# Performance work log

Hardware: AMD Instinct MI355X
Metric: run time of the kernel (lower is better)

The kernel has to match this reference:

```python
import jax, jax.numpy as jnp
import numpy as np

N_QUBITS = 10
CNOT_CHAIN = [(i, i + 1) for i in range(N_QUBITS - 1)] + [(N_QUBITS - 1, 0)]


def setup_inputs() -> dict:
    key = jax.random.key(0)
    k1, k2, k3, k4 = jax.random.split(key, 4)
    B, S, E, F = 32, 512, 1024, 4096
    return {
        "x": jax.random.normal(k1, (B, S, N_QUBITS), dtype=jnp.float32),
        "q_params": jax.random.normal(k2, (N_QUBITS,), dtype=jnp.float32),
        "W1": jax.random.normal(k3, (F, N_QUBITS), dtype=jnp.float32) / np.sqrt(N_QUBITS),
        "W2": jax.random.normal(k4, (E, F), dtype=jnp.float32) / np.sqrt(F),
    }


def _simulate(angles):
    """Batched state-vector sim: RX(angle_i) on wire i from |0..0>, CNOT ring,
    then Pauli-Z expectation on every wire. angles: [N, n] -> [N, n]."""
    N, n = angles.shape
    half = 0.5 * angles
    c, s = jnp.cos(half), jnp.sin(half)
    # RX(theta)|0> = [cos(theta/2), -i sin(theta/2)]; per-qubit states [N, n, 2]
    qs = jnp.stack([c.astype(jnp.complex64), (-1j) * s.astype(jnp.complex64)], axis=-1)
    # product state via iterated Kronecker product -> [N, 2^n]
    state = qs[:, 0]
    for i in range(1, n):
        state = (state[:, :, None] * qs[:, i][:, None, :]).reshape(N, -1)
    state = state.reshape((N,) + (2,) * n)  # axis i+1 <-> wire i
    # CNOT(src, tgt): flip target amplitudes on the control=1 half (permutation)
    for src, tgt in CNOT_CHAIN:
        s0, s1 = jnp.split(state, 2, axis=src + 1)
        state = jnp.concatenate([s0, jnp.flip(s1, axis=tgt + 1)], axis=src + 1)
    probs = (state.real ** 2 + state.imag ** 2).reshape(N, -1)  # [N, 2^n]
    # <Z_i> = sum_k p_k * (1 - 2*bit_i(k)); wire 0 is the most-significant bit
    bits = (jnp.arange(2 ** n)[:, None] >> (n - 1 - jnp.arange(n))) & 1
    signs = (1 - 2 * bits).astype(probs.dtype)  # [2^n, n]
    return probs @ signs


def reference(x, q_params, W1, W2):
    B, S, n = x.shape
    # back-to-back RX on the same wire commute: angles add
    angles = (x + q_params).reshape(B * S, n)
    q_out = _simulate(angles).reshape(B, S, n)
    # dropout is identity at inference; it sits before ReLU and is a no-op here
    h = jax.nn.relu(q_out @ W1.T)  # [B, S, ffn_dim]
    return h @ W2.T  # [B, S, embed_dim]
```

## Files before the change

### kernel.cpp

```cpp
#include <hip/hip_runtime.h>
#include <hip/hip_bf16.h>

typedef __bf16 bf16x8 __attribute__((ext_vector_type(8)));
typedef float f32x16 __attribute__((ext_vector_type(16)));

#define NQ     10
#define M_ROWS 16384
#define N_COLS 1024
#define K_DIM  4096

__device__ __forceinline__ void gload_lds16(const __hip_bfloat16* g, __hip_bfloat16* l) {
  __builtin_amdgcn_global_load_lds(
      (const __attribute__((address_space(1))) void*)g,
      (__attribute__((address_space(3))) void*)l,
      16, 0, 0);
}

__global__ void __launch_bounds__(256) prep(const float* __restrict__ W1,
                                            float* __restrict__ W1T,
                                            const float* __restrict__ W2,
                                            __hip_bfloat16* __restrict__ W2b) {
  const int b = blockIdx.x;
  if (b < 4096) {
    int i = (b * 256 + threadIdx.x) * 4;
    float4 v = *(const float4*)(W2 + i);
    union { __hip_bfloat16 h[4]; uint2 u; } p;
    p.h[0] = __float2bfloat16(v.x);
    p.h[1] = __float2bfloat16(v.y);
    p.h[2] = __float2bfloat16(v.z);
    p.h[3] = __float2bfloat16(v.w);
    *(uint2*)(W2b + i) = p.u;
  } else {
    int f = (b - 4096) * 256 + threadIdx.x;
#pragma unroll
    for (int j = 0; j < NQ; j++)
      W1T[j * K_DIM + f] = W1[f * NQ + j];
  }
}

__global__ void __launch_bounds__(256) compute_h(const float* __restrict__ x,
                                                 const float* __restrict__ qp,
                                                 const float* __restrict__ W1T,
                                                 __hip_bfloat16* __restrict__ h) {
  __shared__ float qs[8][NQ];
  const int tid = threadIdx.x;
  const int r0 = blockIdx.x * 8;

  if (tid < 8 * NQ) {
    int r = tid / NQ, j = tid % NQ;
    qs[r][j] = cosf(x[(r0 + r) * NQ + j] + qp[j]);
  }
  __syncthreads();
  if (tid < 8) {
    float c[NQ];
#pragma unroll
    for (int j = 0; j < NQ; j++) c[j] = qs[tid][j];
    float pref = c[0];
    float prod19 = 1.f;
#pragma unroll
    for (int j = 1; j < NQ; j++) prod19 *= c[j];
    qs[tid][0] = prod19;
#pragma unroll
    for (int k = 1; k < NQ; k++) { pref *= c[k]; qs[tid][k] = pref; }
  }
  __syncthreads();

#pragma unroll 1
  for (int k = 0; k < 2; k++) {
    const int col0 = k * 2048 + tid * 8;
    float w[8][NQ];
#pragma unroll
    for (int j = 0; j < NQ; j++) {
      float4 a = *(const float4*)(W1T + j * K_DIM + col0);
      float4 b = *(const float4*)(W1T + j * K_DIM + col0 + 4);
      w[0][j] = a.x; w[1][j] = a.y; w[2][j] = a.z; w[3][j] = a.w;
      w[4][j] = b.x; w[5][j] = b.y; w[6][j] = b.z; w[7][j] = b.w;
    }
#pragma unroll
    for (int r = 0; r < 8; r++) {
      float q[NQ];
#pragma unroll
      for (int j = 0; j < NQ; j++) q[j] = qs[r][j];
      union { __hip_bfloat16 hh[8]; uint4 u; } pk;
#pragma unroll
      for (int c = 0; c < 8; c++) {
        float acc = 0.f;
#pragma unroll
        for (int j = 0; j < NQ; j++) acc = fmaf(q[j], w[c][j], acc);
        pk.hh[c] = __float2bfloat16(fmaxf(acc, 0.f));
      }
      *(uint4*)(h + (r0 + r) * K_DIM + col0) = pk.u;
    }
  }
}

__global__ void __launch_bounds__(256, 2) gemm_bt(const __hip_bfloat16* __restrict__ A,
                                                  const __hip_bfloat16* __restrict__ B,
                                                  float* __restrict__ C) {
  __shared__ __align__(16) __hip_bfloat16 As[256 * 64];
  __shared__ __align__(16) __hip_bfloat16 Bs[128 * 64];

  const int tid  = threadIdx.x;
  const int wave = tid >> 6;
  const int lane = tid & 63;
  const int l31  = lane & 31;
  const int l5   = lane >> 5;
  const int l7   = l31 & 7;
  const int wm   = (wave & 1) * 128;
  const int wn   = (wave >> 1) * 64;

  const int L    = blockIdx.x;
  const int xcd  = L & 7;
  const int idx  = L >> 3;
  const int col0 = (idx >> 3) * 128;
  const int row0 = ((xcd << 3) | (idx & 7)) * 256;

  const int ldrow = lane >> 3;
  const int ldc   = (((lane & 7) ^ ldrow) << 3);

  f32x16 acc[4][2];
#pragma unroll
  for (int i = 0; i < 4; i++)
#pragma unroll
    for (int j = 0; j < 2; j++)
#pragma unroll
      for (int r = 0; r < 16; r++) acc[i][j][r] = 0.f;

  for (int k0 = 0; k0 < K_DIM; k0 += 64) {
#pragma unroll
    for (int i = 0; i < 8; i++)
      gload_lds16(A + (row0 + wave * 64 + i * 8 + ldrow) * K_DIM + k0 + ldc,
                  As + (wave * 8 + i) * 512);
#pragma unroll
    for (int i = 0; i < 4; i++)
      gload_lds16(B + (col0 + wave * 32 + i * 8 + ldrow) * K_DIM + k0 + ldc,
                  Bs + (wave * 4 + i) * 512);
    __syncthreads();

#pragma unroll
    for (int kki = 0; kki < 4; kki++) {
      const int ch = (((2 * kki + l5) ^ l7) << 3);
      bf16x8 af[4], bb[2];
#pragma unroll
      for (int f = 0; f < 4; f++)
        af[f] = *(const bf16x8*)(As + (wm + f * 32 + l31) * 64 + ch);
#pragma unroll
      for (int f = 0; f < 2; f++)
        bb[f] = *(const bf16x8*)(Bs + (wn + f * 32 + l31) * 64 + ch);
#pragma unroll
      for (int fm = 0; fm < 4; fm++)
#pragma unroll
        for (int fn = 0; fn < 2; fn++)
          acc[fm][fn] = __builtin_amdgcn_mfma_f32_32x32x16_bf16(af[fm], bb[fn], acc[fm][fn], 0, 0, 0);
    }
    __syncthreads();
  }

#pragma unroll
  for (int fm = 0; fm < 4; fm++) {
#pragma unroll
    for (int fn = 0; fn < 2; fn++) {
      const int colb = col0 + wn + fn * 32 + l31;
      const int rowb = row0 + wm + fm * 32 + 4 * l5;
#pragma unroll
      for (int reg = 0; reg < 16; reg++) {
        int row = rowb + (reg & 3) + 8 * (reg >> 2);
        C[row * N_COLS + colb] = acc[fm][fn][reg];
      }
    }
  }
}

extern "C" void kernel_launch(void* const* d_in, const int* in_sizes, int n_in,
                              void* d_out, int out_size, void* d_ws, size_t ws_size,
                              hipStream_t stream) {
  const float* x  = (const float*)d_in[0];
  const float* qp = (const float*)d_in[1];
  const float* W1 = (const float*)d_in[2];
  const float* W2 = (const float*)d_in[3];
  float* out = (float*)d_out;

  char* ws = (char*)d_ws;
  float*          W1T = (float*)ws;
  __hip_bfloat16* W2b = (__hip_bfloat16*)(ws + 163840);
  __hip_bfloat16* hbf = (__hip_bfloat16*)(ws + 163840 + 8388608);

  prep<<<4112, 256, 0, stream>>>(W1, W1T, W2, W2b);
  compute_h<<<M_ROWS / 8, 256, 0, stream>>>(x, qp, W1T, hbf);
  gemm_bt<<<(M_ROWS / 256) * (N_COLS / 128), 256, 0, stream>>>(hbf, W2b, out);
}
```

Before: 248.7 us.

## Fuse first-layer projection into GEMM via MFMA, dropping h materialization

Removes the separate compute_h kernel and the 128MB bf16 h buffer. Inside the GEMM, each k-tile of h is recomputed on the fly with an MFMA (W1 padded to K=16 times the quantum features), passed through ReLU, and written swizzled into LDS. The quantum feature computation moves into the prep kernel, which emits padded bf16 Q and W1 arrays. This trades the global write and read of h for redundant recomputation of h across the 8 column blocks and extra MFMA and LDS-write work per k-step.

```diff
diff --git a/kernel.cpp b/kernel.cpp
--- a/kernel.cpp
+++ b/kernel.cpp
@@ -17,12 +17,16 @@
 }
 
 __global__ void __launch_bounds__(256) prep(const float* __restrict__ W1,
-                                            float* __restrict__ W1T,
                                             const float* __restrict__ W2,
-                                            __hip_bfloat16* __restrict__ W2b) {
+                                            const float* __restrict__ x,
+                                            const float* __restrict__ qp,
+                                            __hip_bfloat16* __restrict__ W2b,
+                                            __hip_bfloat16* __restrict__ Wq,
+                                            __hip_bfloat16* __restrict__ Qb) {
   const int b = blockIdx.x;
+  const int tid = threadIdx.x;
   if (b < 4096) {
-    int i = (b * 256 + threadIdx.x) * 4;
+    int i = (b * 256 + tid) * 4;
     float4 v = *(const float4*)(W2 + i);
     union { __hip_bfloat16 h[4]; uint2 u; } p;
     p.h[0] = __float2bfloat16(v.x);
@@ -30,73 +34,42 @@
     p.h[2] = __float2bfloat16(v.z);
     p.h[3] = __float2bfloat16(v.w);
     *(uint2*)(W2b + i) = p.u;
+  } else if (b < 4112) {
+    int kcol = (b - 4096) * 256 + tid;
+    union { __hip_bfloat16 h[16]; uint4 u[2]; } p;
+#pragma unroll
+    for (int j = 0; j < NQ; j++) p.h[j] = __float2bfloat16(W1[kcol * NQ + j]);
+#pragma unroll
+    for (int j = NQ; j < 16; j++) p.h[j] = __float2bfloat16(0.f);
+    *(uint4*)(Wq + kcol * 16) = p.u[0];
+    *(uint4*)(Wq + kcol * 16 + 8) = p.u[1];
   } else {
-    int f = (b - 4096) * 256 + threadIdx.x;
+    int row = (b - 4112) * 256 + tid;
+    float c[NQ];
 #pragma unroll
-    for (int j = 0; j < NQ; j++)
-      W1T[j * K_DIM + f] = W1[f * NQ + j];
+    for (int j = 0; j < NQ; j++) c[j] = cosf(x[row * NQ + j] + qp[j]);
+    float q[NQ];
+    float prod19 = 1.f;
+#pragma unroll
+    for (int j = 1; j < NQ; j++) prod19 *= c[j];
+    q[0] = prod19;
+    float pref = c[0];
+#pragma unroll
+    for (int k = 1; k < NQ; k++) { pref *= c[k]; q[k] = pref; }
+    union { __hip_bfloat16 h[16]; uint4 u[2]; } p;
+#pragma unroll
+    for (int j = 0; j < NQ; j++) p.h[j] = __float2bfloat16(q[j]);
+#pragma unroll
+    for (int j = NQ; j < 16; j++) p.h[j] = __float2bfloat16(0.f);
+    *(uint4*)(Qb + row * 16) = p.u[0];
+    *(uint4*)(Qb + row * 16 + 8) = p.u[1];
   }
 }
 
-__global__ void __launch_bounds__(256) compute_h(const float* __restrict__ x,
-                                                 const float* __restrict__ qp,
-                                                 const float* __restrict__ W1T,
-                                                 __hip_bfloat16* __restrict__ h) {
-  __shared__ float qs[8][NQ];
-  const int tid = threadIdx.x;
-  const int r0 = blockIdx.x * 8;
-
-  if (tid < 8 * NQ) {
-    int r = tid / NQ, j = tid % NQ;
-    qs[r][j] = cosf(x[(r0 + r) * NQ + j] + qp[j]);
-  }
-  __syncthreads();
-  if (tid < 8) {
-    float c[NQ];
-#pragma unroll
-    for (int j = 0; j < NQ; j++) c[j] = qs[tid][j];
-    float pref = c[0];
-    float prod19 = 1.f;
-#pragma unroll
-    for (int j = 1; j < NQ; j++) prod19 *= c[j];
-    qs[tid][0] = prod19;
-#pragma unroll
-    for (int k = 1; k < NQ; k++) { pref *= c[k]; qs[tid][k] = pref; }
-  }
-  __syncthreads();
-
-#pragma unroll 1
-  for (int k = 0; k < 2; k++) {
-    const int col0 = k * 2048 + tid * 8;
-    float w[8][NQ];
-#pragma unroll
-    for (int j = 0; j < NQ; j++) {
-      float4 a = *(const float4*)(W1T + j * K_DIM + col0);
-      float4 b = *(const float4*)(W1T + j * K_DIM + col0 + 4);
-      w[0][j] = a.x; w[1][j] = a.y; w[2][j] = a.z; w[3][j] = a.w;
-      w[4][j] = b.x; w[5][j] = b.y; w[6][j] = b.z; w[7][j] = b.w;
-    }
-#pragma unroll
-    for (int r = 0; r < 8; r++) {
-      float q[NQ];
-#pragma unroll
-      for (int j = 0; j < NQ; j++) q[j] = qs[r][j];
-      union { __hip_bfloat16 hh[8]; uint4 u; } pk;
-#pragma unroll
-      for (int c = 0; c < 8; c++) {
-        float acc = 0.f;
-#pragma unroll
-        for (int j = 0; j < NQ; j++) acc = fmaf(q[j], w[c][j], acc);
-        pk.hh[c] = __float2bfloat16(fmaxf(acc, 0.f));
-      }
-      *(uint4*)(h + (r0 + r) * K_DIM + col0) = pk.u;
-    }
-  }
-}
-
-__global__ void __launch_bounds__(256, 2) gemm_bt(const __hip_bfloat16* __restrict__ A,
-                                                  const __hip_bfloat16* __restrict__ B,
-                                                  float* __restrict__ C) {
+__global__ void __launch_bounds__(256, 2) gemm_fused(const __hip_bfloat16* __restrict__ Qb,
+                                                     const __hip_bfloat16* __restrict__ Wq,
+                                                     const __hip_bfloat16* __restrict__ B,
+                                                     float* __restrict__ C) {
   __shared__ __align__(16) __hip_bfloat16 As[256 * 64];
   __shared__ __align__(16) __hip_bfloat16 Bs[128 * 64];
 
@@ -118,6 +91,11 @@
   const int ldrow = lane >> 3;
   const int ldc   = (((lane & 7) ^ ldrow) << 3);
 
+  bf16x8 qb[2];
+#pragma unroll
+  for (int i = 0; i < 2; i++)
+    qb[i] = *(const bf16x8*)(Qb + (row0 + (2 * wave + i) * 32 + l31) * 16 + l5 * 8);
+
   f32x16 acc[4][2];
 #pragma unroll
   for (int i = 0; i < 4; i++)
@@ -128,13 +106,35 @@
 
   for (int k0 = 0; k0 < K_DIM; k0 += 64) {
 #pragma unroll
-    for (int i = 0; i < 8; i++)
-      gload_lds16(A + (row0 + wave * 64 + i * 8 + ldrow) * K_DIM + k0 + ldc,
-                  As + (wave * 8 + i) * 512);
-#pragma unroll
     for (int i = 0; i < 4; i++)
       gload_lds16(B + (col0 + wave * 32 + i * 8 + ldrow) * K_DIM + k0 + ldc,
                   Bs + (wave * 4 + i) * 512);
+
+    bf16x8 wq[2];
+#pragma unroll
+    for (int kt = 0; kt < 2; kt++)
+      wq[kt] = *(const bf16x8*)(Wq + (k0 + kt * 32 + l31) * 16 + l5 * 8);
+
+#pragma unroll
+    for (int kt = 0; kt < 2; kt++) {
+#pragma unroll
+      for (int i = 0; i < 2; i++) {
+        f32x16 d;
+#pragma unroll
+        for (int r = 0; r < 16; r++) d[r] = 0.f;
+        d = __builtin_amdgcn_mfma_f32_32x32x16_bf16(wq[kt], qb[i], d, 0, 0, 0);
+        const int hrow = (2 * wave + i) * 32 + l31;
+#pragma unroll
+        for (int q = 0; q < 4; q++) {
+          union { __hip_bfloat16 h[4]; ushort4 u; } p;
+#pragma unroll
+          for (int r = 0; r < 4; r++)
+            p.h[r] = __float2bfloat16(fmaxf(d[4 * q + r], 0.f));
+          const int slot = (kt * 4 + q) ^ (l31 & 7);
+          *(ushort4*)(As + hrow * 64 + slot * 8 + 4 * l5) = p.u;
+        }
+      }
+    }
     __syncthreads();
 
 #pragma unroll
@@ -181,11 +181,10 @@
   float* out = (float*)d_out;
 
   char* ws = (char*)d_ws;
-  float*          W1T = (float*)ws;
-  __hip_bfloat16* W2b = (__hip_bfloat16*)(ws + 163840);
-  __hip_bfloat16* hbf = (__hip_bfloat16*)(ws + 163840 + 8388608);
+  __hip_bfloat16* W2b = (__hip_bfloat16*)ws;
+  __hip_bfloat16* Wq  = (__hip_bfloat16*)(ws + 8388608);
+  __hip_bfloat16* Qb  = (__hip_bfloat16*)(ws + 8519680);
 
-  prep<<<4112, 256, 0, stream>>>(W1, W1T, W2, W2b);
-  compute_h<<<M_ROWS / 8, 256, 0, stream>>>(x, qp, W1T, hbf);
-  gemm_bt<<<(M_ROWS / 256) * (N_COLS / 128), 256, 0, stream>>>(hbf, W2b, out);
+  prep<<<4176, 256, 0, stream>>>(W1, W2, x, qp, W2b, Wq, Qb);
+  gemm_fused<<<(M_ROWS / 256) * (N_COLS / 128), 256, 0, stream>>>(Qb, Wq, W2b, out);
 }
```

New measurement: 225.4 us. 1.1x faster.
